# Kernel optimization log

Hardware: AMD Instinct MI355X
Metric: run time of the kernel (lower is better)

The kernel has to match this reference:

```python
import jax, jax.numpy as jnp
import numpy as np

EPS = 1e-6

def _elu_fm(x):
    # elu(x) + 1 feature map
    return jax.nn.elu(x) + 1.0

def setup_inputs() -> dict:
    key = jax.random.key(0)
    k1, k2, k3, k4, k5 = jax.random.split(key, 5)
    B, N, D, M = 32, 32, 256, 256
    return {
        "query": jax.random.normal(k1, (B, N, D), dtype=jnp.float32),
        "key": jax.random.normal(k2, (B, N, D), dtype=jnp.float32),
        "value": jax.random.normal(k3, (B, N, M), dtype=jnp.float32),
        "Si": jax.random.normal(k4, (B, N, D, M), dtype=jnp.float32) * 0.1,
        "Zi": jax.random.uniform(k5, (B, N, D), dtype=jnp.float32),
    }

def reference(query, key, value, Si, Zi):
    Q = _elu_fm(query)                    # [B,N,D]
    K = _elu_fm(key)                      # [B,N,D]
    Zi_new = Zi + K                       # [B,N,D]
    Si_new = Si + jnp.einsum('bnd,bnm->bndm', K, value)  # [B,N,D,M]
    Z = 1.0 / (jnp.einsum('bnd,bnd->bn', Q, Zi_new) + EPS)  # [B,N]
    V = jnp.einsum('bnd,bndm,bn->bnm', Q, Si_new, Z)      # [B,N,M]
    return (V, Si_new, Zi_new)
```

## Files before the change

kernel.cpp:

```cpp
#include <hip/hip_runtime.h>
#include <math.h>

#define EPS 1e-6f

typedef float f4 __attribute__((ext_vector_type(4)));

__device__ __forceinline__ float elu1(float x) {
    return x > 0.0f ? x + 1.0f : __expf(x);
}

__global__ __launch_bounds__(256) void rla_kernel(
    const float* __restrict__ query,
    const float* __restrict__ key,
    const float* __restrict__ value,
    const float* __restrict__ Si,
    const float* __restrict__ Zi,
    float* __restrict__ V_out,
    float* __restrict__ Si_out,
    float* __restrict__ Zi_out)
{
    const int bn = blockIdx.x;
    const int t  = threadIdx.x;

    __shared__ float sQ[256];
    __shared__ float sK[256];
    __shared__ float red[4 * 256];
    __shared__ float sden[4];
    __shared__ float sZ;

    const size_t base = (size_t)bn * 256;

    float q  = elu1(query[base + t]);
    float k  = elu1(key[base + t]);
    float zn = Zi[base + t] + k;
    Zi_out[base + t] = zn;
    sQ[t] = q;
    sK[t] = k;

    float part = q * zn;
    #pragma unroll
    for (int off = 32; off > 0; off >>= 1)
        part += __shfl_down(part, off, 64);
    if ((t & 63) == 0) sden[t >> 6] = part;
    __syncthreads();
    if (t == 0) {
        float den = sden[0] + sden[1] + sden[2] + sden[3];
        sZ = 1.0f / (den + EPS);
    }

    const int c = t & 63;
    const int w = t >> 6;

    const f4 v = ((const f4*)(value + base))[c];

    const f4* SiB = (const f4*)(Si     + (size_t)bn * 256 * 256) + c;
    f4*       SoB = (f4*)      (Si_out + (size_t)bn * 256 * 256) + c;

    f4 acc = (f4)(0.0f);

    #pragma unroll 4
    for (int d0 = 0; d0 < 256; d0 += 8) {
        const int dA = d0 + w;
        const int dB = dA + 4;
        const float kA = sK[dA];
        const float qA = sQ[dA];
        const float kB = sK[dB];
        const float qB = sQ[dB];
        f4 sa = __builtin_nontemporal_load(SiB + (size_t)dA * 64);
        f4 sb = __builtin_nontemporal_load(SiB + (size_t)dB * 64);
        f4 na = sa + kA * v;
        f4 nb = sb + kB * v;
        __builtin_nontemporal_store(na, SoB + (size_t)dA * 64);
        __builtin_nontemporal_store(nb, SoB + (size_t)dB * 64);
        acc += qA * na;
        acc += qB * nb;
    }

    ((f4*)(red + w * 256))[c] = acc;
    __syncthreads();
    const float vsum = red[0 * 256 + t] + red[1 * 256 + t]
                     + red[2 * 256 + t] + red[3 * 256 + t];
    V_out[base + t] = vsum * sZ;
}

extern "C" void kernel_launch(void* const* d_in, const int* in_sizes, int n_in,
                              void* d_out, int out_size, void* d_ws, size_t ws_size,
                              hipStream_t stream) {
    const float* query = (const float*)d_in[0];
    const float* key_  = (const float*)d_in[1];
    const float* value = (const float*)d_in[2];
    const float* Si    = (const float*)d_in[3];
    const float* Zi    = (const float*)d_in[4];

    const int BN = in_sizes[0] / 256;
    float* V_out  = (float*)d_out;
    float* Si_out = V_out + (size_t)BN * 256;
    float* Zi_out = Si_out + (size_t)BN * 256 * 256;

    rla_kernel<<<BN, 256, 0, stream>>>(query, key_, value, Si, Zi,
                                       V_out, Si_out, Zi_out);
}
```

Baseline: 436.7 us.

## Software-pipeline Si loads with register double-buffering and contiguous per-wave rows

Each wavefront now owns a contiguous block of 64 rows of Si instead of interleaved rows, and Si loads are double-buffered in registers, with 8 rows in flight while the previous 8 are updated and stored. The first batch of Si loads is issued before the elementwise prologue and the reduction barrier, so memory latency overlaps the setup work. This aims to raise memory-level parallelism in a purely bandwidth-bound kernel, at the cost of more vector registers per thread.

```diff
diff --git a/kernel.cpp b/kernel.cpp
--- a/kernel.cpp
+++ b/kernel.cpp
@@ -30,6 +30,20 @@
 
     const size_t base = (size_t)bn * 256;
 
+    const int c = t & 63;
+    const int w = t >> 6;
+    const int row0 = w * 64;
+
+    const f4* SiB = (const f4*)(Si     + (size_t)bn * 65536) + (size_t)row0 * 64 + c;
+    f4*       SoB = (f4*)      (Si_out + (size_t)bn * 65536) + (size_t)row0 * 64 + c;
+
+    f4 cur[8], nxt[8];
+    #pragma unroll
+    for (int j = 0; j < 8; ++j)
+        cur[j] = __builtin_nontemporal_load(SiB + j * 64);
+
+    const f4 v = ((const f4*)(value + base))[c];
+
     float q  = elu1(query[base + t]);
     float k  = elu1(key[base + t]);
     float zn = Zi[base + t] + k;
@@ -48,32 +62,30 @@
         sZ = 1.0f / (den + EPS);
     }
 
-    const int c = t & 63;
-    const int w = t >> 6;
-
-    const f4 v = ((const f4*)(value + base))[c];
-
-    const f4* SiB = (const f4*)(Si     + (size_t)bn * 256 * 256) + c;
-    f4*       SoB = (f4*)      (Si_out + (size_t)bn * 256 * 256) + c;
+    const float* Kp = sK + row0;
+    const float* Qp = sQ + row0;
 
     f4 acc = (f4)(0.0f);
 
-    #pragma unroll 4
-    for (int d0 = 0; d0 < 256; d0 += 8) {
-        const int dA = d0 + w;
-        const int dB = dA + 4;
-        const float kA = sK[dA];
-        const float qA = sQ[dA];
-        const float kB = sK[dB];
-        const float qB = sQ[dB];
-        f4 sa = __builtin_nontemporal_load(SiB + (size_t)dA * 64);
-        f4 sb = __builtin_nontemporal_load(SiB + (size_t)dB * 64);
-        f4 na = sa + kA * v;
-        f4 nb = sb + kB * v;
-        __builtin_nontemporal_store(na, SoB + (size_t)dA * 64);
-        __builtin_nontemporal_store(nb, SoB + (size_t)dB * 64);
-        acc += qA * na;
-        acc += qB * nb;
+    for (int g = 1; g < 8; ++g) {
+        #pragma unroll
+        for (int j = 0; j < 8; ++j)
+            nxt[j] = __builtin_nontemporal_load(SiB + (g * 8 + j) * 64);
+        const int rp = (g - 1) * 8;
+        #pragma unroll
+        for (int j = 0; j < 8; ++j) {
+            f4 n = cur[j] + Kp[rp + j] * v;
+            __builtin_nontemporal_store(n, SoB + (rp + j) * 64);
+            acc += Qp[rp + j] * n;
+        }
+        #pragma unroll
+        for (int j = 0; j < 8; ++j) cur[j] = nxt[j];
+    }
+    #pragma unroll
+    for (int j = 0; j < 8; ++j) {
+        f4 n = cur[j] + Kp[56 + j] * v;
+        __builtin_nontemporal_store(n, SoB + (56 + j) * 64);
+        acc += Qp[56 + j] * n;
     }
 
     ((f4*)(red + w * 256))[c] = acc;
```

Measured after the change: 442.6 us. No clear change (+1.3%).
